# Kernel optimization log

Measured on AMD Instinct MI355X. Metric: run time of the kernel, lower is better.

## Reference

```python
import jax, jax.numpy as jnp
import numpy as np

EMBED_DIM = 1024
LATEN_DIM = 1024
B, S = 4, 2048


def setup_inputs() -> dict:
    key = jax.random.key(0)
    k1, k2, k3, k4, k5 = jax.random.split(key, 5)
    xq = jax.random.normal(k1, (B, S, EMBED_DIM), dtype=jnp.float32)
    xk = jax.random.normal(k2, (B, S, EMBED_DIM), dtype=jnp.float32)
    xv = jax.random.normal(k3, (B, S, EMBED_DIM), dtype=jnp.float32)
    # Linear weight init similar to torch default scale
    bound = 1.0 / np.sqrt(EMBED_DIM)
    Wq = jax.random.uniform(k4, (EMBED_DIM, EMBED_DIM), minval=-bound, maxval=bound, dtype=jnp.float32)
    bq = jax.random.uniform(k5, (EMBED_DIM,), minval=-bound, maxval=bound, dtype=jnp.float32)
    # causal mask: 1 => masked (future positions)
    att_mask = jnp.triu(jnp.ones((S, S), dtype=jnp.int32), k=1)
    return {"xq": xq, "xk": xk, "xv": xv, "Wq": Wq, "bq": bq, "att_mask": att_mask}


def reference(xq, xk, xv, Wq, bq, att_mask):
    scale = LATEN_DIM ** (-0.5)
    # Faithful to source: linearQ is applied to all three inputs.
    Q = jnp.einsum('bsd,ed->bse', xq, Wq) + bq
    K = jnp.einsum('bsd,ed->bse', xk, Wq) + bq
    V = jnp.einsum('bsd,ed->bse', xv, Wq) + bq
    scores = jnp.einsum('bqe,bke->bqk', Q, K) * scale  # [B, S, S]
    scores = jnp.where(att_mask == 1, -jnp.inf, scores)
    probs = jax.nn.softmax(scores, axis=-1)
    return jnp.einsum('bqk,bke->bqe', probs, V)
```

## Files before the change

### kernel.cpp

```cpp
#include <hip/hip_runtime.h>
#include <hip/hip_bf16.h>
#include <stdint.h>


typedef __attribute__((ext_vector_type(8))) short bf16x8;
typedef __attribute__((ext_vector_type(4))) float floatx4;

#define DEVI static __device__ __forceinline__

static constexpr int S_ = 2048;
static constexpr int E_ = 1024;
static constexpr int BATCH = 4;
static constexpr int N4X = 8192 * 1024 / 4;

DEVI unsigned short f2b(float f) {
  union { float f; unsigned u; } v; v.f = f;
  return (unsigned short)((v.u + 0x7FFFu + ((v.u >> 16) & 1u)) >> 16);
}

DEVI void async_load16(const void* g, void* l) {
  __builtin_amdgcn_global_load_lds(
      (__attribute__((address_space(1))) void*)(void*)(g),
      (__attribute__((address_space(3))) void*)(l),
      16, 0, 0);
}

template <int ROWS>
DEVI void stage(const unsigned short* __restrict__ src, int ld,
                unsigned short* ls, int tid) {
#pragma unroll
  for (int j = 0; j < ROWS / 64; ++j) {
    const int u = tid + j * 512;
    const int row = u >> 3, slot = u & 7;
    async_load16(src + row * ld + ((slot ^ (row & 7)) << 3), ls + u * 8);
  }
}

DEVI bf16x8 ldfrag(const unsigned short* ls, int r, int kslot) {
  return *(const bf16x8*)(ls + r * 64 + ((kslot ^ (r & 7)) << 3));
}

template <int NFR>
DEVI void kloop(const unsigned short* __restrict__ A, int lda,
                const unsigned short* __restrict__ Bm, int ldb, int NT,
                unsigned short* lsA, unsigned short* lsB, int tid,
                floatx4 (&acc)[4][NFR]) {
  const int lane = tid & 63;
  const int wr = (tid >> 6) >> 2, wc = (tid >> 6) & 3;
  const int lrow = lane & 15, g = lane >> 4;
  constexpr int BROWS = NFR * 64;
  constexpr int AH = 128 * 64, BH = BROWS * 64;

  stage<128>(A, lda, lsA, tid);
  stage<BROWS>(Bm, ldb, lsB, tid);
  if (NT > 1) {
    stage<128>(A + 64, lda, lsA + AH, tid);
    stage<BROWS>(Bm + 64, ldb, lsB + BH, tid);
  }

  for (int t = 0; t < NT; ++t) {
    const int par = t & 1;
    if (t + 1 < NT) {
      if constexpr (NFR == 4)
        asm volatile("s_waitcnt vmcnt(6)" ::: "memory");
      else
        asm volatile("s_waitcnt vmcnt(4)" ::: "memory");
    } else {
      asm volatile("s_waitcnt vmcnt(0)" ::: "memory");
    }
    asm volatile("s_barrier" ::: "memory");

    const unsigned short* la = lsA + par * AH;
    const unsigned short* lb = lsB + par * BH;
    bf16x8 a[4][2];
#pragma unroll
    for (int mi = 0; mi < 4; ++mi)
#pragma unroll
      for (int ks = 0; ks < 2; ++ks)
        a[mi][ks] = ldfrag(la, wr * 64 + mi * 16 + lrow, g + ks * 4);
#pragma unroll
    for (int nq = 0; nq < NFR / 2; ++nq) {
      bf16x8 b[2][2];
#pragma unroll
      for (int ni = 0; ni < 2; ++ni)
#pragma unroll
        for (int ks = 0; ks < 2; ++ks)
          b[ni][ks] = ldfrag(lb, wc * (NFR * 16) + (nq * 2 + ni) * 16 + lrow,
                             g + ks * 4);
      __builtin_amdgcn_s_setprio(1);
#pragma unroll
      for (int mi = 0; mi < 4; ++mi)
#pragma unroll
        for (int ni = 0; ni < 2; ++ni)
#pragma unroll
          for (int ks = 0; ks < 2; ++ks)
            acc[mi][nq * 2 + ni] = __builtin_amdgcn_mfma_f32_16x16x32_bf16(
                a[mi][ks], b[ni][ks], acc[mi][nq * 2 + ni], 0, 0, 0);
      __builtin_amdgcn_s_setprio(0);
    }
    asm volatile("s_barrier" ::: "memory");
    if (t + 2 < NT) {
      stage<128>(A + (t + 2) * 64, lda, lsA + par * AH, tid);
      stage<BROWS>(Bm + (t + 2) * 64, ldb, lsB + par * BH, tid);
    }
  }
}

__global__ void cvt_all(const float* __restrict__ xq,
                        const float* __restrict__ xk,
                        const float* __restrict__ xv,
                        const float* __restrict__ Wq,
                        unsigned short* __restrict__ Xb,
                        unsigned short* __restrict__ Wb) {
  int i = blockIdx.x * blockDim.x + threadIdx.x;
  const float4* src;
  ushort4* dst;
  if (i < 3 * N4X) {
    int seg = i / N4X, off = i - seg * N4X;
    const float* s = (seg == 0) ? xq : (seg == 1) ? xk : xv;
    src = (const float4*)s + off;
    dst = (ushort4*)(Xb + (size_t)seg * 8192 * 1024) + off;
  } else {
    int off = i - 3 * N4X;
    src = (const float4*)Wq + off;
    dst = (ushort4*)Wb + off;
  }
  float4 v = *src;
  ushort4 o;
  o.x = f2b(v.x); o.y = f2b(v.y); o.z = f2b(v.z); o.w = f2b(v.w);
  *dst = o;
}

__global__ __launch_bounds__(512) void gemm_qkv(
    const unsigned short* __restrict__ Xb, const unsigned short* __restrict__ Wb,
    const float* __restrict__ bias, unsigned short* __restrict__ Qb,
    unsigned short* __restrict__ Kb, unsigned short* __restrict__ Vt) {
  __shared__ __align__(16) unsigned short lsA[2 * 128 * 64];
  __shared__ __align__(16) unsigned short lsB[2 * 256 * 64];
  const int l = blockIdx.x;
  const int xcd = l & 7, i = l >> 3;
  const int gid = xcd * 96 + i;
  const int bn = gid & 3, bmg = gid >> 2;
  const unsigned short* A = Xb + (size_t)bmg * 128 * 1024;
  const unsigned short* W = Wb + (size_t)bn * 256 * 1024;
  const int tid = threadIdx.x;

  floatx4 acc[4][4] = {};
  kloop<4>(A, 1024, W, 1024, 16, lsA, lsB, tid, acc);

  const int lane = tid & 63, wave = tid >> 6;
  const int wr = wave >> 2, wc = wave & 3;
  const int lrow = lane & 15, rb = (lane >> 4) * 4;
  const int input = bmg >> 6;
  unsigned short* C = (input == 0) ? Qb : (input == 1) ? Kb : Vt;
  const int rowbase = (bmg & 63) * 128 + wr * 64;
#pragma unroll
  for (int mi = 0; mi < 4; ++mi)
#pragma unroll
    for (int ni = 0; ni < 4; ++ni) {
      const int gcol = bn * 256 + wc * 64 + ni * 16 + lrow;
      const float bv = bias[gcol];
#pragma unroll
      for (int r = 0; r < 4; ++r) {
        const int grow = rowbase + mi * 16 + rb + r;
        const unsigned short val = f2b(acc[mi][ni][r] + bv);
        if (input == 2) {
          int b = grow >> 11, s = grow & 2047;
          C[((size_t)b * 1024 + gcol) * 2048 + s] = val;
        } else {
          C[(size_t)grow * 1024 + gcol] = val;
        }
      }
    }
}

__global__ __launch_bounds__(512) void gemm_scores_exp(
    const unsigned short* __restrict__ Qb,
    const unsigned short* __restrict__ Kb, unsigned short* __restrict__ P,
    float* __restrict__ lsum) {
  __shared__ __align__(16) unsigned short lsA[2 * 128 * 64];
  __shared__ __align__(16) unsigned short lsB[2 * 256 * 64];
  const int l = blockIdx.x;
  const int xcd = l & 7, i = l >> 3;
  const int gid = xcd * 36 + i;
  const int z = gid / 72;
  int r0 = gid % 72;
  int bm = 0;
  for (;;) { const int c = (bm >> 1) + 1; if (r0 < c) break; r0 -= c; ++bm; }
  const int bnn = r0;

  const unsigned short* A = Qb + ((size_t)z * S_ + bm * 128) * E_;
  const unsigned short* Bt = Kb + ((size_t)z * S_ + bnn * 256) * E_;
  const int tid = threadIdx.x;

  floatx4 acc[4][4] = {};
  kloop<4>(A, E_, Bt, E_, 16, lsA, lsB, tid, acc);

  const int lane = tid & 63, wave = tid >> 6;
  const int wr = wave >> 2, wc = wave & 3;
  const int lrow = lane & 15, rb = (lane >> 4) * 4;
  const bool diag = (bnn == (bm >> 1));
#pragma unroll
  for (int mi = 0; mi < 4; ++mi)
#pragma unroll
    for (int r = 0; r < 4; ++r) {
      const int grow = bm * 128 + wr * 64 + mi * 16 + rb + r;
      float rsum = 0.f;
#pragma unroll
      for (int ni = 0; ni < 4; ++ni) {
        const int gcol = bnn * 256 + wc * 64 + ni * 16 + lrow;
        float p = __expf(acc[mi][ni][r] * 0.03125f);
        if (diag && gcol > grow) p = 0.f;
        P[((size_t)z * S_ + grow) * S_ + gcol] = f2b(p);
        rsum += p;
      }
#pragma unroll
      for (int off = 1; off < 16; off <<= 1) rsum += __shfl_xor(rsum, off);
      if ((lane & 15) == 0) atomicAdd(&lsum[z * S_ + grow], rsum);
    }
}

__global__ __launch_bounds__(512) void gemm_pv(
    const unsigned short* __restrict__ Pb,
    const unsigned short* __restrict__ Vt, const float* __restrict__ lsum,
    float* __restrict__ Out) {
  __shared__ __align__(16) unsigned short lsA[2 * 128 * 64];
  __shared__ __align__(16) unsigned short lsB[2 * 128 * 64];
  const int l = blockIdx.x;
  const int xcd = l & 7, i = l >> 3;
  const int bn = i & 7, j = i >> 3;
  const int z = j >> 1;
  const int bm = (j & 1) ? xcd : 15 - xcd;

  const unsigned short* A = Pb + ((size_t)z * S_ + bm * 128) * S_;
  const unsigned short* Bt = Vt + ((size_t)z * E_ + bn * 128) * S_;
  float* C = Out + (size_t)z * S_ * E_;
  const int tid = threadIdx.x;
  const int NT = 2 * bm + 2;

  floatx4 acc[4][2] = {};
  kloop<2>(A, S_, Bt, S_, NT, lsA, lsB, tid, acc);

  const int lane = tid & 63, wave = tid >> 6;
  const int wr = wave >> 2, wc = wave & 3;
  const int lrow = lane & 15, rb = (lane >> 4) * 4;
#pragma unroll
  for (int mi = 0; mi < 4; ++mi)
#pragma unroll
    for (int r = 0; r < 4; ++r) {
      const int grow = bm * 128 + wr * 64 + mi * 16 + rb + r;
      const float inv = 1.0f / lsum[z * S_ + grow];
#pragma unroll
      for (int ni = 0; ni < 2; ++ni) {
        const int gcol = bn * 128 + wc * 32 + ni * 16 + lrow;
        C[(size_t)grow * E_ + gcol] = acc[mi][ni][r] * inv;
      }
    }
}

extern "C" void kernel_launch(void* const* d_in, const int* in_sizes, int n_in,
                              void* d_out, int out_size, void* d_ws,
                              size_t ws_size, hipStream_t stream) {
  (void)in_sizes; (void)n_in; (void)out_size; (void)ws_size;
  const float* xq = (const float*)d_in[0];
  const float* xk = (const float*)d_in[1];
  const float* xv = (const float*)d_in[2];
  const float* Wq = (const float*)d_in[3];
  const float* bq = (const float*)d_in[4];
  float* out = (float*)d_out;

  unsigned short* base16 = (unsigned short*)d_ws;
  unsigned short* Xb = base16;
  unsigned short* P = base16;
  unsigned short* Wb = base16 + (size_t)24 * 1024 * 1024;
  unsigned short* Qb = Wb + (size_t)1024 * 1024;
  unsigned short* Kb = Qb + (size_t)8192 * 1024;
  unsigned short* Vt = Kb + (size_t)8192 * 1024;
  float* lsum = (float*)(Vt + (size_t)8192 * 1024);

  hipMemsetAsync(lsum, 0, BATCH * S_ * sizeof(float), stream);

  const int n4tot = 3 * N4X + 1024 * 1024 / 4;
  cvt_all<<<n4tot / 256, 256, 0, stream>>>(xq, xk, xv, Wq, Xb, Wb);

  gemm_qkv<<<768, 512, 0, stream>>>(Xb, Wb, bq, Qb, Kb, Vt);
  gemm_scores_exp<<<288, 512, 0, stream>>>(Qb, Kb, P, lsum);
  gemm_pv<<<512, 512, 0, stream>>>(P, Vt, lsum, out);
}
```

Before: 336.7 us.

## Enlarge GEMM tiles to 256x256 and interleave LDS reads with MFMA quads

Switches the QKV and scores GEMMs to 256x256 block tiles and the PV GEMM to 128x256 tiles. The k-loop is restructured into four MFMA quadrants with fragment reads for the next quadrant issued between barriers, reusing A and B fragments. Grids shrink accordingly. The intent is more reuse of each LDS and global load and overlap of LDS reads with MFMA work. The cost is more registers and LDS per block, fewer blocks (for example 144 for scores), and many extra barriers.

```diff
diff --git a/kernel.cpp b/kernel.cpp
--- a/kernel.cpp
+++ b/kernel.cpp
@@ -40,69 +40,86 @@
   return *(const bf16x8*)(ls + r * 64 + ((kslot ^ (r & 7)) << 3));
 }
 
-template <int NFR>
-DEVI void kloop(const unsigned short* __restrict__ A, int lda,
-                const unsigned short* __restrict__ Bm, int ldb, int NT,
-                unsigned short* lsA, unsigned short* lsB, int tid,
-                floatx4 (&acc)[4][NFR]) {
+template <int N>
+DEVI void read_frags(bf16x8 (&dst)[N][2], const unsigned short* ls, int row0,
+                     int g) {
+#pragma unroll
+  for (int i = 0; i < N; ++i)
+#pragma unroll
+    for (int ks = 0; ks < 2; ++ks)
+      dst[i][ks] = ldfrag(ls, row0 + i * 16, g + ks * 4);
+}
+
+template <int MH, int MO, int NO, int MFR>
+DEVI void quad(bf16x8 (&a)[MH][2], bf16x8 (&b)[2][2], floatx4 (&acc)[MFR][4]) {
+  __builtin_amdgcn_s_setprio(1);
+#pragma unroll
+  for (int mi = 0; mi < MH; ++mi)
+#pragma unroll
+    for (int ni = 0; ni < 2; ++ni)
+#pragma unroll
+      for (int ks = 0; ks < 2; ++ks)
+        acc[MO + mi][NO + ni] = __builtin_amdgcn_mfma_f32_16x16x32_bf16(
+            a[mi][ks], b[ni][ks], acc[MO + mi][NO + ni], 0, 0, 0);
+  __builtin_amdgcn_s_setprio(0);
+}
+
+#define BARRIER asm volatile("s_barrier" ::: "memory")
+#define LGKM0 asm volatile("s_waitcnt lgkmcnt(0)" ::: "memory")
+
+template <int MFR>
+DEVI void kloop4(const unsigned short* __restrict__ A, int lda,
+                 const unsigned short* __restrict__ Bm, int ldb, int NT,
+                 unsigned short* lsA, unsigned short* lsB, int tid,
+                 floatx4 (&acc)[MFR][4]) {
+  constexpr int BM = MFR * 32;
+  constexpr int MH = MFR / 2;
+  constexpr int AH = BM * 64, BH = 256 * 64;
   const int lane = tid & 63;
   const int wr = (tid >> 6) >> 2, wc = (tid >> 6) & 3;
-  const int lrow = lane & 15, g = lane >> 4;
-  constexpr int BROWS = NFR * 64;
-  constexpr int AH = 128 * 64, BH = BROWS * 64;
-
-  stage<128>(A, lda, lsA, tid);
-  stage<BROWS>(Bm, ldb, lsB, tid);
+  const int g = lane >> 4;
+  const int arow0 = wr * (MFR * 16) + (lane & 15);
+  const int brow0 = wc * 64 + (lane & 15);
+
+  stage<BM>(A, lda, lsA, tid);
+  stage<256>(Bm, ldb, lsB, tid);
   if (NT > 1) {
-    stage<128>(A + 64, lda, lsA + AH, tid);
-    stage<BROWS>(Bm + 64, ldb, lsB + BH, tid);
+    stage<BM>(A + 64, lda, lsA + AH, tid);
+    stage<256>(Bm + 64, ldb, lsB + BH, tid);
   }
 
   for (int t = 0; t < NT; ++t) {
     const int par = t & 1;
     if (t + 1 < NT) {
-      if constexpr (NFR == 4)
+      if constexpr (MFR == 8)
+        asm volatile("s_waitcnt vmcnt(8)" ::: "memory");
+      else
         asm volatile("s_waitcnt vmcnt(6)" ::: "memory");
-      else
-        asm volatile("s_waitcnt vmcnt(4)" ::: "memory");
     } else {
       asm volatile("s_waitcnt vmcnt(0)" ::: "memory");
     }
-    asm volatile("s_barrier" ::: "memory");
-
+    BARRIER;
     const unsigned short* la = lsA + par * AH;
     const unsigned short* lb = lsB + par * BH;
-    bf16x8 a[4][2];
-#pragma unroll
-    for (int mi = 0; mi < 4; ++mi)
-#pragma unroll
-      for (int ks = 0; ks < 2; ++ks)
-        a[mi][ks] = ldfrag(la, wr * 64 + mi * 16 + lrow, g + ks * 4);
-#pragma unroll
-    for (int nq = 0; nq < NFR / 2; ++nq) {
-      bf16x8 b[2][2];
-#pragma unroll
-      for (int ni = 0; ni < 2; ++ni)
-#pragma unroll
-        for (int ks = 0; ks < 2; ++ks)
-          b[ni][ks] = ldfrag(lb, wc * (NFR * 16) + (nq * 2 + ni) * 16 + lrow,
-                             g + ks * 4);
-      __builtin_amdgcn_s_setprio(1);
-#pragma unroll
-      for (int mi = 0; mi < 4; ++mi)
-#pragma unroll
-        for (int ni = 0; ni < 2; ++ni)
-#pragma unroll
-          for (int ks = 0; ks < 2; ++ks)
-            acc[mi][nq * 2 + ni] = __builtin_amdgcn_mfma_f32_16x16x32_bf16(
-                a[mi][ks], b[ni][ks], acc[mi][nq * 2 + ni], 0, 0, 0);
-      __builtin_amdgcn_s_setprio(0);
-    }
-    asm volatile("s_barrier" ::: "memory");
+    bf16x8 a[MH][2], b0[2][2], b1[2][2];
+    read_frags<MH>(a, la, arow0, g);
+    read_frags<2>(b0, lb, brow0, g);
+    BARRIER; LGKM0;
+    quad<MH, 0, 0, MFR>(a, b0, acc);
+    BARRIER;
+    read_frags<2>(b1, lb, brow0 + 32, g);
+    BARRIER; LGKM0;
+    quad<MH, 0, 2, MFR>(a, b1, acc);
+    BARRIER;
+    read_frags<MH>(a, la, arow0 + MH * 16, g);
+    BARRIER; LGKM0;
+    quad<MH, MH, 2, MFR>(a, b1, acc);
+    BARRIER;
     if (t + 2 < NT) {
-      stage<128>(A + (t + 2) * 64, lda, lsA + par * AH, tid);
-      stage<BROWS>(Bm + (t + 2) * 64, ldb, lsB + par * BH, tid);
-    }
+      stage<BM>(A + (t + 2) * 64, lda, lsA + par * AH, tid);
+      stage<256>(Bm + (t + 2) * 64, ldb, lsB + par * BH, tid);
+    }
+    quad<MH, MH, 0, MFR>(a, b0, acc);
   }
 }
 
@@ -131,31 +148,31 @@
   *dst = o;
 }
 
-__global__ __launch_bounds__(512) void gemm_qkv(
+__global__ __launch_bounds__(512, 2) void gemm_qkv(
     const unsigned short* __restrict__ Xb, const unsigned short* __restrict__ Wb,
     const float* __restrict__ bias, unsigned short* __restrict__ Qb,
     unsigned short* __restrict__ Kb, unsigned short* __restrict__ Vt) {
-  __shared__ __align__(16) unsigned short lsA[2 * 128 * 64];
+  __shared__ __align__(16) unsigned short lsA[2 * 256 * 64];
   __shared__ __align__(16) unsigned short lsB[2 * 256 * 64];
   const int l = blockIdx.x;
   const int xcd = l & 7, i = l >> 3;
-  const int gid = xcd * 96 + i;
-  const int bn = gid & 3, bmg = gid >> 2;
-  const unsigned short* A = Xb + (size_t)bmg * 128 * 1024;
+  const int bn = i & 3;
+  const int bmg = xcd * 12 + (i >> 2);
+  const unsigned short* A = Xb + (size_t)bmg * 256 * 1024;
   const unsigned short* W = Wb + (size_t)bn * 256 * 1024;
   const int tid = threadIdx.x;
 
-  floatx4 acc[4][4] = {};
-  kloop<4>(A, 1024, W, 1024, 16, lsA, lsB, tid, acc);
+  floatx4 acc[8][4] = {};
+  kloop4<8>(A, 1024, W, 1024, 16, lsA, lsB, tid, acc);
 
   const int lane = tid & 63, wave = tid >> 6;
   const int wr = wave >> 2, wc = wave & 3;
   const int lrow = lane & 15, rb = (lane >> 4) * 4;
-  const int input = bmg >> 6;
+  const int input = bmg / 32;
   unsigned short* C = (input == 0) ? Qb : (input == 1) ? Kb : Vt;
-  const int rowbase = (bmg & 63) * 128 + wr * 64;
-#pragma unroll
-  for (int mi = 0; mi < 4; ++mi)
+  const int rowbase = (bmg % 32) * 256 + wr * 128;
+#pragma unroll
+  for (int mi = 0; mi < 8; ++mi)
 #pragma unroll
     for (int ni = 0; ni < 4; ++ni) {
       const int gcol = bn * 256 + wc * 64 + ni * 16 + lrow;
@@ -174,37 +191,37 @@
     }
 }
 
-__global__ __launch_bounds__(512) void gemm_scores_exp(
+__global__ __launch_bounds__(512, 2) void gemm_scores_exp(
     const unsigned short* __restrict__ Qb,
     const unsigned short* __restrict__ Kb, unsigned short* __restrict__ P,
     float* __restrict__ lsum) {
-  __shared__ __align__(16) unsigned short lsA[2 * 128 * 64];
+  __shared__ __align__(16) unsigned short lsA[2 * 256 * 64];
   __shared__ __align__(16) unsigned short lsB[2 * 256 * 64];
   const int l = blockIdx.x;
   const int xcd = l & 7, i = l >> 3;
-  const int gid = xcd * 36 + i;
-  const int z = gid / 72;
-  int r0 = gid % 72;
+  const int gid = xcd * 18 + i;
+  const int z = gid / 36;
+  int r0 = gid % 36;
   int bm = 0;
-  for (;;) { const int c = (bm >> 1) + 1; if (r0 < c) break; r0 -= c; ++bm; }
+  for (;;) { const int c = bm + 1; if (r0 < c) break; r0 -= c; ++bm; }
   const int bnn = r0;
 
-  const unsigned short* A = Qb + ((size_t)z * S_ + bm * 128) * E_;
+  const unsigned short* A = Qb + ((size_t)z * S_ + bm * 256) * E_;
   const unsigned short* Bt = Kb + ((size_t)z * S_ + bnn * 256) * E_;
   const int tid = threadIdx.x;
 
-  floatx4 acc[4][4] = {};
-  kloop<4>(A, E_, Bt, E_, 16, lsA, lsB, tid, acc);
+  floatx4 acc[8][4] = {};
+  kloop4<8>(A, E_, Bt, E_, 16, lsA, lsB, tid, acc);
 
   const int lane = tid & 63, wave = tid >> 6;
   const int wr = wave >> 2, wc = wave & 3;
   const int lrow = lane & 15, rb = (lane >> 4) * 4;
-  const bool diag = (bnn == (bm >> 1));
-#pragma unroll
-  for (int mi = 0; mi < 4; ++mi)
+  const bool diag = (bnn == bm);
+#pragma unroll
+  for (int mi = 0; mi < 8; ++mi)
 #pragma unroll
     for (int r = 0; r < 4; ++r) {
-      const int grow = bm * 128 + wr * 64 + mi * 16 + rb + r;
+      const int grow = bm * 256 + wr * 128 + mi * 16 + rb + r;
       float rsum = 0.f;
 #pragma unroll
       for (int ni = 0; ni < 4; ++ni) {
@@ -220,26 +237,26 @@
     }
 }
 
-__global__ __launch_bounds__(512) void gemm_pv(
+__global__ __launch_bounds__(512, 2) void gemm_pv(
     const unsigned short* __restrict__ Pb,
     const unsigned short* __restrict__ Vt, const float* __restrict__ lsum,
     float* __restrict__ Out) {
   __shared__ __align__(16) unsigned short lsA[2 * 128 * 64];
-  __shared__ __align__(16) unsigned short lsB[2 * 128 * 64];
+  __shared__ __align__(16) unsigned short lsB[2 * 256 * 64];
   const int l = blockIdx.x;
   const int xcd = l & 7, i = l >> 3;
-  const int bn = i & 7, j = i >> 3;
+  const int bn = i & 3, j = i >> 2;
   const int z = j >> 1;
   const int bm = (j & 1) ? xcd : 15 - xcd;
 
   const unsigned short* A = Pb + ((size_t)z * S_ + bm * 128) * S_;
-  const unsigned short* Bt = Vt + ((size_t)z * E_ + bn * 128) * S_;
+  const unsigned short* Bt = Vt + ((size_t)z * E_ + bn * 256) * S_;
   float* C = Out + (size_t)z * S_ * E_;
   const int tid = threadIdx.x;
   const int NT = 2 * bm + 2;
 
-  floatx4 acc[4][2] = {};
-  kloop<2>(A, S_, Bt, S_, NT, lsA, lsB, tid, acc);
+  floatx4 acc[4][4] = {};
+  kloop4<4>(A, S_, Bt, S_, NT, lsA, lsB, tid, acc);
 
   const int lane = tid & 63, wave = tid >> 6;
   const int wr = wave >> 2, wc = wave & 3;
@@ -251,8 +268,8 @@
       const int grow = bm * 128 + wr * 64 + mi * 16 + rb + r;
       const float inv = 1.0f / lsum[z * S_ + grow];
 #pragma unroll
-      for (int ni = 0; ni < 2; ++ni) {
-        const int gcol = bn * 128 + wc * 32 + ni * 16 + lrow;
+      for (int ni = 0; ni < 4; ++ni) {
+        const int gcol = bn * 256 + wc * 64 + ni * 16 + lrow;
         C[(size_t)grow * E_ + gcol] = acc[mi][ni][r] * inv;
       }
     }
@@ -283,7 +300,7 @@
   const int n4tot = 3 * N4X + 1024 * 1024 / 4;
   cvt_all<<<n4tot / 256, 256, 0, stream>>>(xq, xk, xv, Wq, Xb, Wb);
 
-  gemm_qkv<<<768, 512, 0, stream>>>(Xb, Wb, bq, Qb, Kb, Vt);
-  gemm_scores_exp<<<288, 512, 0, stream>>>(Qb, Kb, P, lsum);
-  gemm_pv<<<512, 512, 0, stream>>>(P, Vt, lsum, out);
-}
+  gemm_qkv<<<384, 512, 0, stream>>>(Xb, Wb, bq, Qb, Kb, Vt);
+  gemm_scores_exp<<<144, 512, 0, stream>>>(Qb, Kb, P, lsum);
+  gemm_pv<<<256, 512, 0, stream>>>(P, Vt, lsum, out);
+}
```

Result: slower. 353.0 us (+4.8%).
